# Kernel optimization log

Measured on AMD Instinct MI355X. Metric: run time of the kernel, lower is better.

## Reference

```python
import jax, jax.numpy as jnp
import numpy as np

KS = 5          # kernel_size
D = 2           # spatial dim
DX = 0.01       # region kernel spacing
SCALE = 1.0
NX, NY = 32, 32
N = NX * NY


def _region_kernel():
    # gaussians.region_kernel: KS x KS grid of offsets spaced DX, centered at 0
    off = (jnp.arange(KS, dtype=jnp.float32) - (KS - 1) / 2.0) * DX
    gx, gy = jnp.meshgrid(off, off, indexing='ij')
    return jnp.stack([gx, gy], -1).reshape(-1, D)  # (KS*KS, 2)


def _build_cov(scaling, transform):
    # Cholesky-style parameterization: L lower-triangular with diag=scaling,
    # off-diag=transform; cov = L @ L^T (d=2 closed form)
    s0, s1 = scaling[:, 0], scaling[:, 1]
    t = transform[:, 0]
    c00 = s0 * s0
    c01 = s0 * t
    c11 = t * t + s1 * s1
    return jnp.stack([jnp.stack([c00, c01], -1), jnp.stack([c01, c11], -1)], -2)


def _inv2x2(c):
    det = c[:, 0, 0] * c[:, 1, 1] - c[:, 0, 1] * c[:, 1, 0]
    inv = jnp.stack([jnp.stack([c[:, 1, 1], -c[:, 0, 1]], -1),
                     jnp.stack([-c[:, 1, 0], c[:, 0, 0]], -1)], -2)
    return inv / det[:, None, None]


def setup_inputs() -> dict:
    key = jax.random.key(0)
    ks = jax.random.split(key, 20)
    # Gaussian state: grid means as in __init__
    tx = jnp.linspace(-1.0, 1.0, NX) * SCALE
    ty = jnp.linspace(-1.0, 1.0, NY) * SCALE
    gx, gy = jnp.meshgrid(tx, ty, indexing='ij')
    means = jnp.stack([gx, gy], -1).reshape(-1, D).astype(jnp.float32)
    u = 0.1 * jax.random.normal(ks[0], (N, 1), jnp.float32)
    scaling = jnp.exp(-4.5 + 0.2 * jax.random.normal(ks[1], (N, D), jnp.float32)) * SCALE
    transform = 0.002 * jax.random.normal(ks[2], (N, 1), jnp.float32)
    opacities = 2.0 + 0.1 * jax.random.normal(ks[3], (N,), jnp.float32)
    # network weights (4 heads share the first 3 layer shapes)
    convW = 0.05 * jax.random.normal(ks[4], (4, 50, 3, KS, KS), jnp.float32)
    convb = 0.01 * jax.random.normal(ks[5], (4, 50), jnp.float32)
    embW = 0.3 * jax.random.normal(ks[6], (4, 7, 30), jnp.float32)
    embb = 0.01 * jax.random.normal(ks[7], (4, 30), jnp.float32)
    l1W = 0.1 * jax.random.normal(ks[8], (4, 80, 80), jnp.float32)
    l1b = 0.01 * jax.random.normal(ks[9], (4, 80), jnp.float32)
    outW_sol = 0.1 * jax.random.normal(ks[10], (80, 1), jnp.float32)
    outb_sol = 0.01 * jax.random.normal(ks[11], (1,), jnp.float32)
    outW_trans = 0.1 * jax.random.normal(ks[12], (80, 2), jnp.float32)
    outb_trans = 0.01 * jax.random.normal(ks[13], (2,), jnp.float32)
    outW_scale = 0.1 * jax.random.normal(ks[14], (80, 2), jnp.float32)
    outb_scale = 0.01 * jax.random.normal(ks[15], (2,), jnp.float32)
    outW_tform = 0.1 * jax.random.normal(ks[16], (80, 1), jnp.float32)
    outb_tform = 0.01 * jax.random.normal(ks[17], (1,), jnp.float32)
    return {"means": means, "u": u, "scaling": scaling, "transform": transform,
            "opacities": opacities, "convW": convW, "convb": convb,
            "embW": embW, "embb": embb, "l1W": l1W, "l1b": l1b,
            "outW_sol": outW_sol, "outb_sol": outb_sol,
            "outW_trans": outW_trans, "outb_trans": outb_trans,
            "outW_scale": outW_scale, "outb_scale": outb_scale,
            "outW_tform": outW_tform, "outb_tform": outb_tform}


def reference(means, u, scaling, transform, opacities, convW, convb, embW, embb,
              l1W, l1b, outW_sol, outb_sol, outW_trans, outb_trans,
              outW_scale, outb_scale, outW_tform, outb_tform):
    n = means.shape[0]
    cov = _build_cov(scaling, transform)          # (N,2,2)
    conics = _inv2x2(cov)                         # (N,2,2)

    # --- sampling (torch.no_grad block in original) ---
    kern = _region_kernel()                                        # (25,2)
    samples = (means[:, None, :] + kern[None]).reshape(-1, D)      # (M,2), M=N*25
    bc = jnp.all(jnp.abs(samples) < SCALE, -1).astype(means.dtype)[:, None]
    alpha = jax.nn.sigmoid(opacities)                              # (N,)
    diff = samples[:, None, :] - means[None, :, :]                 # (M,N,2)
    Cq = jnp.einsum('nij,mnj->mni', conics, diff)                  # (M,N,2)
    G = jnp.exp(-0.5 * jnp.einsum('mni,mni->mn', diff, Cq)) * alpha[None, :]  # (M,N)
    u_s = G @ u                                                    # (M,1)
    # DIFFUSION pde_rhs = trace of laplacian: sum_n G * (|C q|^2 - tr(C)) * u_n
    trC = conics[:, 0, 0] + conics[:, 1, 1]
    lap = jnp.einsum('mn,mn,nc->mc', G, (Cq ** 2).sum(-1) - trC[None, :], u)  # (M,1)
    in_samples = jax.lax.stop_gradient(jnp.concatenate([u_s, lap, bc], -1))   # (M,3)

    # (N, 25, 3) -> (N, 3, 5, 5)
    img = in_samples.reshape(n, KS * KS, -1).transpose(0, 2, 1).reshape(n, -1, KS, KS)
    in_params = jnp.concatenate([means, u, scaling, transform, opacities[:, None]], -1)  # (N,7)

    # 4 Networks: conv(5x5 -> 1x1, 50ch) + param embed(7->30) + MLP(80->80->out)
    y = jnp.tanh(jnp.einsum('ncij,kocij->kno', img, convW) + convb[:, None, :])   # (4,N,50)
    e = jnp.tanh(jnp.einsum('nf,kfg->kng', in_params, embW) + embb[:, None, :])   # (4,N,30)
    h = jnp.tanh(jnp.einsum('knf,kfg->kng', jnp.concatenate([y, e], -1), l1W)
                 + l1b[:, None, :])                                               # (4,N,80)

    deltas = h[0] @ outW_sol + outb_sol          # (N,1)
    translation = h[1] @ outW_trans + outb_trans # (N,2)
    dscale = h[2] @ outW_scale + outb_scale      # (N,2)
    dtransform = h[3] @ outW_tform + outb_tform  # (N,1)

    u_new = u + deltas
    means_new = means + translation
    scaling_new = scaling * jnp.exp(dscale)
    transform_new = transform + dtransform
    cov_new = _build_cov(scaling_new, transform_new)
    return (u_new, means_new, scaling_new, transform_new, cov_new)
```

## Files before the change

kernel.cpp:

```cpp
#include <hip/hip_runtime.h>
#include <hip/hip_bf16.h>


#define NG 1024

__device__ __forceinline__ float tanh_fast(float x) {
    return 1.0f - 2.0f / (__expf(2.0f * x) + 1.0f);
}

__global__ __launch_bounds__(256) void k_fused(
    const float* __restrict__ means, const float* __restrict__ u,
    const float* __restrict__ scal, const float* __restrict__ trans,
    const float* __restrict__ opac,
    const float* __restrict__ convW, const float* __restrict__ convb,
    const float* __restrict__ embW,  const float* __restrict__ embb,
    const float* __restrict__ l1W,   const float* __restrict__ l1b,
    const float* __restrict__ oWs,  const float* __restrict__ obs,
    const float* __restrict__ oWt,  const float* __restrict__ obt,
    const float* __restrict__ oWsc, const float* __restrict__ obsc,
    const float* __restrict__ oWtf, const float* __restrict__ obtf,
    float* __restrict__ out)
{
    __shared__ float gcomp[NG * 8];
    __shared__ float pus[2][4][32];
    __shared__ float plap[2][4][32];
    __shared__ float simg[2][80];
    __shared__ float hin[2][4][80];
    __shared__ float hv[2][4][80];
    __shared__ float outs[2][8];
    __shared__ int   cnt;

    const int t  = threadIdx.x;
    const int n0 = blockIdx.x * 2;
    const float mx0 = means[2*n0],   my0 = means[2*n0+1];
    const float mx1 = means[2*n0+2], my1 = means[2*n0+3];
    const float bxmin = fminf(mx0, mx1) - 0.02f, bxmax = fmaxf(mx0, mx1) + 0.02f;
    const float bymin = fminf(my0, my1) - 0.02f, bymax = fmaxf(my0, my1) + 0.02f;

    if (t == 0) cnt = 0;
    __syncthreads();
    for (int g = t; g < NG; g += 256) {
        float gmx = means[2*g], gmy = means[2*g+1];
        float s0  = scal[2*g],  s1  = scal[2*g+1];
        float tt  = trans[g];
        float c00 = s0*s0, c01 = s0*tt, c11 = tt*tt + s1*s1;
        float r2  = 100.0f * (c00 + c11);
        float ddx = fmaxf(fmaxf(bxmin - gmx, gmx - bxmax), 0.0f);
        float ddy = fmaxf(fmaxf(bymin - gmy, gmy - bymax), 0.0f);
        if (ddx*ddx + ddy*ddy <= r2) {
            float idet = 1.0f / (c00*c11 - c01*c01);
            float A = c11*idet, B = -c01*idet, C = c00*idet;
            float alpha = 1.0f / (1.0f + __expf(-opac[g]));
            int slot = atomicAdd(&cnt, 1);
            float4* dst = (float4*)(gcomp + slot*8);
            dst[0] = make_float4(gmx, gmy, A, B);
            dst[1] = make_float4(C, A + C, alpha * u[g], 0.0f);
        }
    }
    __syncthreads();
    const int nsurv = cnt;

    {
        int c = t >> 6, lane = t & 63, l = lane >> 5, s = lane & 31;
        if (s < 25) {
            int si = s / 5, sj = s - si * 5;
            float gx = l ? mx1 : mx0, gy = l ? my1 : my0;
            float sx = gx + (float)(si - 2) * 0.01f;
            float sy = gy + (float)(sj - 2) * 0.01f;
            float us = 0.0f, lp = 0.0f;
            #pragma unroll 2
            for (int i = c; i < nsurv; i += 4) {
                float4 a = *(const float4*)(gcomp + i*8);
                float4 b = *(const float4*)(gcomp + i*8 + 4);
                float dx = sx - a.x, dy = sy - a.y;
                float Cq0 = a.z*dx + a.w*dy;
                float Cq1 = a.w*dx + b.x*dy;
                float q   = dx*Cq0 + dy*Cq1;
                float e   = __expf(-0.5f*q) * b.z;
                us += e;
                lp += e * (Cq0*Cq0 + Cq1*Cq1 - b.y);
            }
            pus[l][c][s] = us; plap[l][c][s] = lp;
        }
    }
    __syncthreads();

    if (t < 50) {
        int l = t / 25, s = t - l * 25;
        float us = 0.0f, lp = 0.0f;
        #pragma unroll
        for (int c = 0; c < 4; ++c) { us += pus[l][c][s]; lp += plap[l][c][s]; }
        int si = s / 5, sj = s - si * 5;
        float gx = l ? mx1 : mx0, gy = l ? my1 : my0;
        float sx = gx + (float)(si - 2) * 0.01f;
        float sy = gy + (float)(sj - 2) * 0.01f;
        simg[l][s]      = us;
        simg[l][25 + s] = lp;
        simg[l][50 + s] = (fabsf(sx) < 1.0f && fabsf(sy) < 1.0f) ? 1.0f : 0.0f;
    }
    __syncthreads();

    if (t < 200) {
        const float* w = convW + (size_t)t * 75;
        float a0 = convb[t], a1 = a0;
        #pragma unroll 5
        for (int j = 0; j < 75; ++j) {
            float wj = w[j];
            a0 += simg[0][j] * wj;
            a1 += simg[1][j] * wj;
        }
        int k = t / 50, o = t - k * 50;
        hin[0][k][o] = tanh_fast(a0);
        hin[1][k][o] = tanh_fast(a1);
    } else {
        for (int idx = t - 200; idx < 240; idx += 56) {
            int l = idx / 120, rem = idx - l * 120;
            int k = rem / 30, g = rem - k * 30;
            int n = n0 + l;
            float inp[7] = { means[2*n], means[2*n+1], u[n], scal[2*n],
                             scal[2*n+1], trans[n], opac[n] };
            float acc = embb[k * 30 + g];
            #pragma unroll
            for (int f = 0; f < 7; ++f) acc += inp[f] * embW[(k*7 + f)*30 + g];
            hin[l][k][50 + g] = tanh_fast(acc);
        }
    }
    __syncthreads();

    for (int p = t; p < 320; p += 256) {
        int k = p / 80, g = p - k * 80;
        float a0 = l1b[p], a1 = a0;
        #pragma unroll 8
        for (int f = 0; f < 80; ++f) {
            float w = l1W[(k*80 + f)*80 + g];
            a0 += hin[0][k][f] * w;
            a1 += hin[1][k][f] * w;
        }
        hv[0][k][g] = tanh_fast(a0);
        hv[1][k][g] = tanh_fast(a1);
    }
    __syncthreads();

    if (t < 12) {
        int l = t / 6, t6 = t - l * 6;
        const float* W; const float* bb; int k, j, stride;
        if (t6 == 0)      { W = oWs;  bb = obs;  k = 0; j = 0;      stride = 1; }
        else if (t6 < 3)  { W = oWt;  bb = obt;  k = 1; j = t6 - 1; stride = 2; }
        else if (t6 < 5)  { W = oWsc; bb = obsc; k = 2; j = t6 - 3; stride = 2; }
        else              { W = oWtf; bb = obtf; k = 3; j = 0;      stride = 1; }
        float acc = bb[j];
        #pragma unroll 8
        for (int f = 0; f < 80; ++f) acc += hv[l][k][f] * W[f * stride + j];
        outs[l][t6] = acc;
    }
    __syncthreads();

    if (t < 2) {
        int n = n0 + t;
        float uu = u[n];
        float s0 = scal[2*n], s1 = scal[2*n+1];
        float tr = trans[n];
        float u_new = uu + outs[t][0];
        float mxn = (t ? mx1 : mx0) + outs[t][1];
        float myn = (t ? my1 : my0) + outs[t][2];
        float s0n = s0 * __expf(outs[t][3]);
        float s1n = s1 * __expf(outs[t][4]);
        float tn  = tr + outs[t][5];
        float c00 = s0n*s0n, c01 = s0n*tn, c11 = tn*tn + s1n*s1n;
        out[n]              = u_new;
        out[1024 + 2*n]     = mxn;
        out[1024 + 2*n + 1] = myn;
        out[3072 + 2*n]     = s0n;
        out[3072 + 2*n + 1] = s1n;
        out[5120 + n]       = tn;
        out[6144 + 4*n]     = c00;
        out[6144 + 4*n + 1] = c01;
        out[6144 + 4*n + 2] = c01;
        out[6144 + 4*n + 3] = c11;
    }
}

extern "C" void kernel_launch(void* const* d_in, const int* in_sizes, int n_in,
                              void* d_out, int out_size, void* d_ws, size_t ws_size,
                              hipStream_t stream)
{
    k_fused<<<dim3(NG / 2), dim3(256), 0, stream>>>(
        (const float*)d_in[0],  (const float*)d_in[1],  (const float*)d_in[2],
        (const float*)d_in[3],  (const float*)d_in[4],  (const float*)d_in[5],
        (const float*)d_in[6],  (const float*)d_in[7],  (const float*)d_in[8],
        (const float*)d_in[9],  (const float*)d_in[10], (const float*)d_in[11],
        (const float*)d_in[12], (const float*)d_in[13], (const float*)d_in[14],
        (const float*)d_in[15], (const float*)d_in[16], (const float*)d_in[17],
        (const float*)d_in[18], (float*)d_out);
}
```

Measured before the change: 108.0 us.

## Prefetch MLP weights into registers and restructure per-sample reduction

Conv and first-layer MLP weights are now loaded into per-thread register arrays at kernel start, so their global-memory latency overlaps the gaussian culling phase. The gaussian-evaluation phase is remapped so every lane of every wave works, with a cross-half wave shuffle reduction in place of a 4-way shared-memory reduction. The output-head and final write stages are merged using wave shuffles, which removes one barrier and a shared buffer. The cost is about 155 extra live floats per thread, which raises register pressure and can lower occupancy or cause spills.

New measurement: 106.4 us. About the same (-1.5%).

```diff
diff --git a/kernel.cpp b/kernel.cpp
--- a/kernel.cpp
+++ b/kernel.cpp
@@ -22,16 +22,32 @@
     float* __restrict__ out)
 {
     __shared__ float gcomp[NG * 8];
-    __shared__ float pus[2][4][32];
-    __shared__ float plap[2][4][32];
+    __shared__ float pus[2][2][32];
+    __shared__ float plap[2][2][32];
     __shared__ float simg[2][80];
     __shared__ float hin[2][4][80];
     __shared__ float hv[2][4][80];
-    __shared__ float outs[2][8];
     __shared__ int   cnt;
 
     const int t  = threadIdx.x;
     const int n0 = blockIdx.x * 2;
+
+    float wcv[75];
+    {
+        const float* w = convW + (size_t)(t < 200 ? t : 0) * 75;
+        #pragma unroll
+        for (int j = 0; j < 75; ++j) wcv[j] = w[j];
+    }
+    float w1[80];
+    {
+        int k = t / 80, g = t - (t / 80) * 80;
+        const float* w = l1W + (size_t)(k * 80) * 80 + g;
+        #pragma unroll
+        for (int f = 0; f < 80; ++f) w1[f] = w[f * 80];
+    }
+    float bcv = (t < 200) ? convb[t] : 0.0f;
+    float b1  = l1b[t];
+
     const float mx0 = means[2*n0],   my0 = means[2*n0+1];
     const float mx1 = means[2*n0+2], my1 = means[2*n0+3];
     const float bxmin = fminf(mx0, mx1) - 0.02f, bxmax = fmaxf(mx0, mx1) + 0.02f;
@@ -61,35 +77,39 @@
     const int nsurv = cnt;
 
     {
-        int c = t >> 6, lane = t & 63, l = lane >> 5, s = lane & 31;
-        if (s < 25) {
-            int si = s / 5, sj = s - si * 5;
-            float gx = l ? mx1 : mx0, gy = l ? my1 : my0;
-            float sx = gx + (float)(si - 2) * 0.01f;
-            float sy = gy + (float)(sj - 2) * 0.01f;
-            float us = 0.0f, lp = 0.0f;
-            #pragma unroll 2
-            for (int i = c; i < nsurv; i += 4) {
-                float4 a = *(const float4*)(gcomp + i*8);
-                float4 b = *(const float4*)(gcomp + i*8 + 4);
-                float dx = sx - a.x, dy = sy - a.y;
-                float Cq0 = a.z*dx + a.w*dy;
-                float Cq1 = a.w*dx + b.x*dy;
-                float q   = dx*Cq0 + dy*Cq1;
-                float e   = __expf(-0.5f*q) * b.z;
-                us += e;
-                lp += e * (Cq0*Cq0 + Cq1*Cq1 - b.y);
-            }
-            pus[l][c][s] = us; plap[l][c][s] = lp;
+        int w = t >> 6, lane = t & 63;
+        int l = w >> 1;
+        int hc = ((w & 1) << 1) | (lane >> 5);
+        int s  = lane & 31; if (s > 24) s = 24;
+        int si = s / 5, sj = s - si * 5;
+        float gx = l ? mx1 : mx0, gy = l ? my1 : my0;
+        float sx = gx + (float)(si - 2) * 0.01f;
+        float sy = gy + (float)(sj - 2) * 0.01f;
+        float us = 0.0f, lp = 0.0f;
+        #pragma unroll 2
+        for (int i = hc; i < nsurv; i += 4) {
+            float4 a = *(const float4*)(gcomp + i*8);
+            float4 b = *(const float4*)(gcomp + i*8 + 4);
+            float dx = sx - a.x, dy = sy - a.y;
+            float Cq0 = a.z*dx + a.w*dy;
+            float Cq1 = a.w*dx + b.x*dy;
+            float q   = dx*Cq0 + dy*Cq1;
+            float e   = __expf(-0.5f*q) * b.z;
+            us += e;
+            lp += e * (Cq0*Cq0 + Cq1*Cq1 - b.y);
+        }
+        us += __shfl_down(us, 32);
+        lp += __shfl_down(lp, 32);
+        if ((lane & 31) == s && lane < 32) {
+            pus[l][w & 1][s] = us; plap[l][w & 1][s] = lp;
         }
     }
     __syncthreads();
 
     if (t < 50) {
         int l = t / 25, s = t - l * 25;
-        float us = 0.0f, lp = 0.0f;
-        #pragma unroll
-        for (int c = 0; c < 4; ++c) { us += pus[l][c][s]; lp += plap[l][c][s]; }
+        float us = pus[l][0][s] + pus[l][1][s];
+        float lp = plap[l][0][s] + plap[l][1][s];
         int si = s / 5, sj = s - si * 5;
         float gx = l ? mx1 : mx0, gy = l ? my1 : my0;
         float sx = gx + (float)(si - 2) * 0.01f;
@@ -101,13 +121,11 @@
     __syncthreads();
 
     if (t < 200) {
-        const float* w = convW + (size_t)t * 75;
-        float a0 = convb[t], a1 = a0;
-        #pragma unroll 5
+        float a0 = bcv, a1 = bcv;
+        #pragma unroll
         for (int j = 0; j < 75; ++j) {
-            float wj = w[j];
-            a0 += simg[0][j] * wj;
-            a1 += simg[1][j] * wj;
+            a0 += simg[0][j] * wcv[j];
+            a1 += simg[1][j] * wcv[j];
         }
         int k = t / 50, o = t - k * 50;
         hin[0][k][o] = tanh_fast(a0);
@@ -127,22 +145,33 @@
     }
     __syncthreads();
 
-    for (int p = t; p < 320; p += 256) {
-        int k = p / 80, g = p - k * 80;
-        float a0 = l1b[p], a1 = a0;
+    {
+        int k = t / 80, g = t - (t / 80) * 80;
+        float a0 = b1, a1 = b1;
+        #pragma unroll
+        for (int f = 0; f < 80; ++f) {
+            a0 += hin[0][k][f] * w1[f];
+            a1 += hin[1][k][f] * w1[f];
+        }
+        hv[0][k][g] = tanh_fast(a0);
+        hv[1][k][g] = tanh_fast(a1);
+    }
+    if (t < 64) {
+        int g = 16 + t;
+        float a0 = l1b[240 + g], a1 = a0;
         #pragma unroll 8
         for (int f = 0; f < 80; ++f) {
-            float w = l1W[(k*80 + f)*80 + g];
-            a0 += hin[0][k][f] * w;
-            a1 += hin[1][k][f] * w;
-        }
-        hv[0][k][g] = tanh_fast(a0);
-        hv[1][k][g] = tanh_fast(a1);
-    }
-    __syncthreads();
-
-    if (t < 12) {
-        int l = t / 6, t6 = t - l * 6;
+            float w = l1W[(3*80 + f)*80 + g];
+            a0 += hin[0][3][f] * w;
+            a1 += hin[1][3][f] * w;
+        }
+        hv[0][3][g] = tanh_fast(a0);
+        hv[1][3][g] = tanh_fast(a1);
+    }
+    __syncthreads();
+
+    if (t < 64) {
+        int l = (t / 6) & 1, t6 = t % 6;
         const float* W; const float* bb; int k, j, stride;
         if (t6 == 0)      { W = oWs;  bb = obs;  k = 0; j = 0;      stride = 1; }
         else if (t6 < 3)  { W = oWt;  bb = obt;  k = 1; j = t6 - 1; stride = 2; }
@@ -151,32 +180,38 @@
         float acc = bb[j];
         #pragma unroll 8
         for (int f = 0; f < 80; ++f) acc += hv[l][k][f] * W[f * stride + j];
-        outs[l][t6] = acc;
-    }
-    __syncthreads();
-
-    if (t < 2) {
-        int n = n0 + t;
-        float uu = u[n];
-        float s0 = scal[2*n], s1 = scal[2*n+1];
-        float tr = trans[n];
-        float u_new = uu + outs[t][0];
-        float mxn = (t ? mx1 : mx0) + outs[t][1];
-        float myn = (t ? my1 : my0) + outs[t][2];
-        float s0n = s0 * __expf(outs[t][3]);
-        float s1n = s1 * __expf(outs[t][4]);
-        float tn  = tr + outs[t][5];
-        float c00 = s0n*s0n, c01 = s0n*tn, c11 = tn*tn + s1n*s1n;
-        out[n]              = u_new;
-        out[1024 + 2*n]     = mxn;
-        out[1024 + 2*n + 1] = myn;
-        out[3072 + 2*n]     = s0n;
-        out[3072 + 2*n + 1] = s1n;
-        out[5120 + n]       = tn;
-        out[6144 + 4*n]     = c00;
-        out[6144 + 4*n + 1] = c01;
-        out[6144 + 4*n + 2] = c01;
-        out[6144 + 4*n + 3] = c11;
+
+        int base = (t / 6) * 6;
+        float o0 = __shfl(acc, base + 0);
+        float o1 = __shfl(acc, base + 1);
+        float o2 = __shfl(acc, base + 2);
+        float o3 = __shfl(acc, base + 3);
+        float o4 = __shfl(acc, base + 4);
+        float o5 = __shfl(acc, base + 5);
+
+        if (t == 0 || t == 6) {
+            int n = n0 + (t / 6);
+            float uu = u[n];
+            float s0 = scal[2*n], s1 = scal[2*n+1];
+            float tr = trans[n];
+            float u_new = uu + o0;
+            float mxn = (t ? mx1 : mx0) + o1;
+            float myn = (t ? my1 : my0) + o2;
+            float s0n = s0 * __expf(o3);
+            float s1n = s1 * __expf(o4);
+            float tn  = tr + o5;
+            float c00 = s0n*s0n, c01 = s0n*tn, c11 = tn*tn + s1n*s1n;
+            out[n]              = u_new;
+            out[1024 + 2*n]     = mxn;
+            out[1024 + 2*n + 1] = myn;
+            out[3072 + 2*n]     = s0n;
+            out[3072 + 2*n + 1] = s1n;
+            out[5120 + n]       = tn;
+            out[6144 + 4*n]     = c00;
+            out[6144 + 4*n + 1] = c01;
+            out[6144 + 4*n + 2] = c01;
+            out[6144 + 4*n + 3] = c11;
+        }
     }
 }
 
```
